# Performance work log

Measured on AMD Instinct MI355X. Metric: run time of the kernel, lower is better.

Reference implementation:

```python
import jax, jax.numpy as jnp
import numpy as np
import math
from jax import lax

# cfg['MODEL'] constants
MU = 0.1          # FISTA step size
LMBD = 0.1        # LAMBDA[0], sparsity weight
N_DICT = 1        # EXPANSION_FACTOR
N_STEPS = 6       # NUM_LAYERS (FISTA iterations)
K = 3             # kernel_size
PAD = 1           # padding
STRIDE = 1        # stride (POOLING=False, stride passed to conv)
DN = ('NCHW', 'OIHW', 'NCHW')


def _conv(x, w):
    # F.conv2d(x, w, stride=1, padding=PAD)
    return lax.conv_general_dilated(x, w, (STRIDE, STRIDE), [(PAD, PAD), (PAD, PAD)], dimension_numbers=DN)


def _conv_t(y, w):
    # F.conv_transpose2d(y, w, stride=1, padding=PAD) == conv2d with flipped, in/out-swapped kernel, pad K-1-PAD
    wt = jnp.transpose(jnp.flip(w, (-1, -2)), (1, 0, 2, 3))  # [Cin, Cout, K, K]
    p = K - 1 - PAD
    return lax.conv_general_dilated(y, wt, (1, 1), [(p, p), (p, p)], dimension_numbers=DN)


def _shrink(z, thr):
    # non_negative=True soft-threshold: relu(z - thr)
    return jax.nn.relu(z - thr)


def setup_inputs() -> dict:
    key = jax.random.key(0)
    k1, k2 = jax.random.split(key)
    x = jax.random.normal(k1, (16, 64, 56, 56), dtype=jnp.float32)
    # dictionary weight [out_channels, in_channels*n_dict, K, K], kaiming-ish scale
    W = jax.random.normal(k2, (128, 64 * N_DICT, K, K), dtype=jnp.float32) * 0.05
    return {"x": x, "W": W}


def reference(x, W):
    # w_norm: each output filter normalized to unit Frobenius norm
    Wn = W / jnp.sqrt(jnp.sum(W * W, axis=(1, 2, 3), keepdims=True) + 1e-12)
    thr = MU * LMBD
    xr = jnp.tile(x, (1, N_DICT, 1, 1)) if N_DICT > 1 else x

    # FISTA iteration 0: c = shrink(mu * D^T x)
    c = _shrink(MU * _conv(xr, Wn), thr)
    y = c
    c_prev = c
    t = 1.0
    for _ in range(N_STEPS - 1):
        r = xr - _conv_t(y, Wn)                       # residual x - D c
        c_new = _shrink(y + MU * _conv(r, Wn), thr)   # gradient step + shrink
        t_next = (1.0 + math.sqrt(1.0 + 4.0 * t * t)) / 2.0
        y = c_new + ((t - 1.0) / t_next) * (c_new - c_prev)  # momentum
        c_prev = c_new
        t = t_next
    # POOLING=False -> DictConv2d returns the sparse code directly
    return c_prev
```

## Files before the change

### kernel.cpp

```cpp
#include <hip/hip_runtime.h>
#include <hip/hip_bf16.h>
#include <math.h>

typedef __attribute__((ext_vector_type(8))) short short8;
typedef __attribute__((ext_vector_type(4))) float f32x4;

#define MU_  0.1f
#define THR_ 0.01f

static __device__ inline short f2bf(float f) {
    __hip_bfloat16 h = __float2bfloat16(f);
    return *reinterpret_cast<short*>(&h);
}
static __device__ inline float bf2f(unsigned short u) {
    unsigned int x = ((unsigned int)u) << 16;
    return __builtin_bit_cast(float, x);
}

#define ZB_ 5916

__global__ __launch_bounds__(256) void prep_kernel(
    const float* __restrict__ x, const float* __restrict__ W,
    float4* __restrict__ zbase, int n4,
    short* __restrict__ Xp, short* __restrict__ Wf2, short* __restrict__ Wt2) {
    __shared__ float lx[64 * 57];
    const int bid = blockIdx.x, tid = threadIdx.x;
    if (bid < ZB_) {
        int i = bid * 256 + tid;
        if (i < n4) zbase[i] = make_float4(0.f, 0.f, 0.f, 0.f);
    } else if (bid < ZB_ + 32) {
        int co = (bid - ZB_) * 4 + (tid >> 6);
        int ci = tid & 63;
        const float* wp = W + (co * 64 + ci) * 9;
        float v[9]; float s = 0.f;
#pragma unroll
        for (int t = 0; t < 9; ++t) { v[t] = wp[t]; s += v[t] * v[t]; }
#pragma unroll
        for (int off = 32; off; off >>= 1) s += __shfl_xor(s, off, 64);
        float inv = 1.0f / sqrtf(s + 1e-12f);
#pragma unroll
        for (int t = 0; t < 9; ++t) {
            Wf2[((t * 8 + (ci >> 3)) * 128 + co) * 8 + (ci & 7)] = f2bf(v[t] * inv);
            Wt2[((t * 16 + (co >> 3)) * 64 + ci) * 8 + (co & 7)] = f2bf(v[8 - t] * inv);
        }
    } else {
        int pb = bid - ZB_ - 32;
        int row = pb % 58, n = pb / 58;
        short* dst = Xp + ((size_t)(n * 58 + row) * 68) * 64;
        if (row >= 1 && row <= 56) {
            int h = row - 1;
            for (int j = tid; j < 64 * 56; j += 256) {
                int ci = j / 56, w = j - ci * 56;
                lx[ci * 57 + w] = x[((size_t)(n * 64 + ci)) * 3136 + h * 56 + w];
            }
            __syncthreads();
            for (int j = tid; j < 68 * 64; j += 256) {
                int s = j >> 6, ci = j & 63;
                float val = (s >= 2 && s < 58) ? lx[ci * 57 + (s - 2)] : 0.f;
                dst[(s << 6) + (ci ^ ((s & 7) << 3))] = f2bf(val);
            }
        } else {
            for (int j = tid; j < 68 * 64; j += 256) dst[j] = 0;
        }
    }
}

__global__ __launch_bounds__(256, 4) void conv_fwd(
    const short* __restrict__ inp,
    const short* __restrict__ Wf2,
    short* __restrict__ Yp,
    short* __restrict__ Cp,
    float* __restrict__ outp, int mode, float beta) {
    __shared__ __align__(16) short smem[14688];
    const int bid = blockIdx.x, tid = threadIdx.x;
    const int sid = (bid & 7) * 112 + (bid >> 3);
    const int n = sid / 56, r = sid - n * 56 + 1;
    {
        const short8* src = (const short8*)(inp + ((size_t)(n * 58 + (r - 1)) * 68) * 64);
        for (int j = tid; j < 1632; j += 256) {
            int srow = j >> 3, w = j & 7;
            *(short8*)(smem + srow * 72 + w * 8) = src[j];
        }
    }
    const int lane = tid & 63, ct = tid >> 6, quad = lane >> 4, l15 = lane & 15;
    const int cog = ct & 1, pxg = ct >> 1;
    const size_t prow = ((size_t)(n * 58 + r) * 68) * 128;

    short8 yold8[2], cold8[2];
    int pvv[2], pg[2]; bool pok[2];
#pragma unroll
    for (int k = 0; k < 2; ++k) {
        int item = tid + k * 256;
        pok[k] = item < 448;
        pvv[k] = item >> 3; pg[k] = item & 7;
        if (mode != 0 && pok[k]) {
            int s = pvv[k] + 2;
            size_t off = prow + (size_t)s * 128 + 8 * (pg[k] ^ (s & 7));
            yold8[k] = *(const short8*)(Yp + off);
            if (mode == 1) cold8[k] = *(const short8*)(Cp + off);
        }
    }
    __syncthreads();

    f32x4 acc[2][4];
#pragma unroll
    for (int pt = 0; pt < 2; ++pt)
#pragma unroll
        for (int cot = 0; cot < 4; ++cot) acc[pt][cot] = (f32x4){0.f, 0.f, 0.f, 0.f};

#pragma unroll
    for (int f = 0; f < 18; ++f) {
        const int t = f >> 1, half = f & 1;
        const int dh = t / 3, dw = t % 3;
        const int u = l15 + dw + 1;
        const int phys = (half * 4 + quad) ^ (u & 7);
        short8 areg[4];
#pragma unroll
        for (int cot = 0; cot < 4; ++cot) {
            const int co = cog * 64 + cot * 16 + l15;
            areg[cot] = *(const short8*)(Wf2 +
                ((size_t)((t * 8 + half * 4 + quad) * 128 + co)) * 8);
        }
#pragma unroll
        for (int pt = 0; pt < 2; ++pt) {
            const int pti = pxg * 2 + pt;
            const short8 bv = *(const short8*)(smem +
                (dh * 68 + pti * 16 + u) * 72 + phys * 8);
#pragma unroll
            for (int cot = 0; cot < 4; ++cot)
                acc[pt][cot] = __builtin_amdgcn_mfma_f32_16x16x32_bf16(areg[cot], bv, acc[pt][cot], 0, 0, 0);
        }
    }

    __syncthreads();
    short* tb_y = smem;
    short* tb_c = smem + 4608;
    const int h = r - 1;
#pragma unroll
    for (int hh = 0; hh < 2; ++hh) {
        if (mode != 0) {
#pragma unroll
            for (int k = 0; k < 2; ++k) if (pok[k]) {
                int o = pvv[k] * 72 + 8 * (pg[k] ^ (pvv[k] & 3));
                *(short8*)(tb_y + o) = yold8[k];
                if (mode == 1) *(short8*)(tb_c + o) = cold8[k];
            }
        }
        __syncthreads();
        if (hh == 0 && mode != 0) {
#pragma unroll
            for (int k = 0; k < 2; ++k) if (pok[k]) {
                int s = pvv[k] + 2;
                size_t off = prow + (size_t)s * 128 + 8 * ((pg[k] + 8) ^ (s & 7));
                yold8[k] = *(const short8*)(Yp + off);
                if (mode == 1) cold8[k] = *(const short8*)(Cp + off);
            }
        }
        if (cog == hh) {
#pragma unroll
            for (int pt = 0; pt < 2; ++pt) {
                const int px = pxg * 32 + pt * 16 + l15;
#pragma unroll
                for (int cot = 0; cot < 4; ++cot) {
#pragma unroll
                    for (int reg = 0; reg < 4; ++reg) {
                        const int lch = cot * 16 + quad * 4 + reg;
                        const int slot = px * 72 + (lch ^ ((px & 3) << 3));
                        const float a = acc[pt][cot][reg];
                        if (mode == 0) {
                            float c = fmaxf(MU_ * a - THR_, 0.f);
                            short cb16 = f2bf(c);
                            tb_y[slot] = cb16;
                            tb_c[slot] = cb16;
                        } else if (mode == 1) {
                            float yold = bf2f((unsigned short)tb_y[slot]);
                            float cold = bf2f((unsigned short)tb_c[slot]);
                            float c = fmaxf(yold + MU_ * a - THR_, 0.f);
                            tb_y[slot] = f2bf(c + beta * (c - cold));
                            tb_c[slot] = f2bf(c);
                        } else {
                            if (px < 56) {
                                float yold = bf2f((unsigned short)tb_y[slot]);
                                float c = fmaxf(yold + MU_ * a - THR_, 0.f);
                                outp[((size_t)(n * 128 + hh * 64 + lch)) * 3136 + h * 56 + px] = c;
                            }
                        }
                    }
                }
            }
        }
        if (mode != 2) {
            __syncthreads();
            for (int item = tid; item < 448; item += 256) {
                int vv = item >> 3, g = item & 7;
                int so = vv * 72 + 8 * (g ^ (vv & 3));
                short8 yv = *(const short8*)(tb_y + so);
                short8 cv = *(const short8*)(tb_c + so);
                int s = vv + 2;
                size_t off = prow + (size_t)s * 128 + 8 * ((g + 8 * hh) ^ (s & 7));
                *(short8*)(Yp + off) = yv;
                *(short8*)(Cp + off) = cv;
            }
        }
        if (hh == 0) __syncthreads();
    }
}

__global__ __launch_bounds__(256, 4) void conv_t(
    const short* __restrict__ Ypb,
    const short* __restrict__ Wt2,
    const short* __restrict__ Xp,
    short* __restrict__ Rp) {
    __shared__ __align__(16) short smem[14688];
    const int bid = blockIdx.x, tid = threadIdx.x;
    const int sid = (bid & 7) * 112 + (bid >> 3);
    const int n = sid / 56, r = sid - n * 56 + 1;
    const int lane = tid & 63, ct = tid >> 6, quad = lane >> 4, l15 = lane & 15;
    const short8* src = (const short8*)(Ypb + ((size_t)(n * 58 + (r - 1)) * 68) * 128);
    const size_t prow = ((size_t)(n * 58 + r) * 68) * 64;

    short8 xold8[2];
    int pvv[2], pg[2]; bool pok[2];
#pragma unroll
    for (int k = 0; k < 2; ++k) {
        int item = tid + k * 256;
        pok[k] = item < 448;
        pvv[k] = item >> 3; pg[k] = item & 7;
        if (pok[k]) {
            int s = pvv[k] + 2;
            xold8[k] = *(const short8*)(Xp + prow + (size_t)s * 64 + 8 * (pg[k] ^ (s & 7)));
        }
    }

    f32x4 acc[4];
#pragma unroll
    for (int cit = 0; cit < 4; ++cit) acc[cit] = (f32x4){0.f, 0.f, 0.f, 0.f};

#pragma unroll
    for (int p = 0; p < 2; ++p) {
        if (p) __syncthreads();
        for (int j = tid; j < 1632; j += 256) {
            int srow = j >> 3, w = j & 7;
            *(short8*)(smem + srow * 72 + w * 8) = src[srow * 16 + p * 8 + w];
        }
        __syncthreads();
#pragma unroll
        for (int f = 0; f < 18; ++f) {
            const int t = f >> 1, sh = f & 1;
            const int dh = t / 3, dw = t % 3;
            const int u = l15 + dw + 1;
            const int phys = (sh * 4 + quad) ^ (u & 7);
            short8 areg[4];
#pragma unroll
            for (int cit = 0; cit < 4; ++cit) {
                const int ci = cit * 16 + l15;
                areg[cit] = *(const short8*)(Wt2 +
                    ((size_t)((t * 16 + (p * 2 + sh) * 4 + quad) * 64 + ci)) * 8);
            }
            const short8 bv = *(const short8*)(smem +
                (dh * 68 + ct * 16 + u) * 72 + phys * 8);
#pragma unroll
            for (int cit = 0; cit < 4; ++cit)
                acc[cit] = __builtin_amdgcn_mfma_f32_16x16x32_bf16(areg[cit], bv, acc[cit], 0, 0, 0);
        }
    }

    __syncthreads();
    short* tb = smem;
#pragma unroll
    for (int k = 0; k < 2; ++k) if (pok[k]) {
        *(short8*)(tb + pvv[k] * 72 + 8 * (pg[k] ^ (pvv[k] & 3))) = xold8[k];
    }
    __syncthreads();
    {
        const int px = ct * 16 + l15;
#pragma unroll
        for (int cit = 0; cit < 4; ++cit) {
#pragma unroll
            for (int reg = 0; reg < 4; ++reg) {
                const int cir = cit * 16 + quad * 4 + reg;
                const int slot = px * 72 + (cir ^ ((px & 3) << 3));
                float xo = bf2f((unsigned short)tb[slot]);
                tb[slot] = f2bf(xo - acc[cit][reg]);
            }
        }
    }
    __syncthreads();
    for (int item = tid; item < 448; item += 256) {
        int vv = item >> 3, g = item & 7;
        short8 val = *(const short8*)(tb + vv * 72 + 8 * (g ^ (vv & 3)));
        int s = vv + 2;
        *(short8*)(Rp + prow + (size_t)s * 64 + 8 * (g ^ (s & 7))) = val;
    }
}

extern "C" void kernel_launch(void* const* d_in, const int* in_sizes, int n_in,
                              void* d_out, int out_size, void* d_ws, size_t ws_size,
                              hipStream_t stream) {
    const float* x = (const float*)d_in[0];
    const float* W = (const float*)d_in[1];
    float* out = (float*)d_out;

    const size_t XPN = (size_t)16 * 58 * 68 * 64;
    const size_t YPN = 2 * XPN;
    short* Xp = (short*)d_ws;
    short* Rp = Xp + XPN;
    short* Yp = Rp + XPN;
    short* Cp = Yp + YPN;
    short* Wf2 = Cp + YPN;
    short* Wt2 = Wf2 + 73728;

    const int n4 = (int)((XPN + YPN) * 2 / 16);
    const int prep_blocks = ZB_ + 32 + 58 * 16;
    hipLaunchKernelGGL(prep_kernel, dim3(prep_blocks), dim3(256), 0, stream,
                       x, W, (float4*)Rp, n4, Xp, Wf2, Wt2);

    dim3 b(256, 1, 1);
    hipLaunchKernelGGL(conv_fwd, dim3(896), b, 0, stream, Xp, Wf2, Yp, Cp,
                       (float*)nullptr, 0, 0.f);
    double t = 1.0;
    for (int it = 1; it <= 5; ++it) {
        hipLaunchKernelGGL(conv_t, dim3(896), b, 0, stream, Yp, Wt2, Xp, Rp);
        double tn = (1.0 + sqrt(1.0 + 4.0 * t * t)) / 2.0;
        float beta = (float)((t - 1.0) / tn);
        hipLaunchKernelGGL(conv_fwd, dim3(896), b, 0, stream, Rp, Wf2, Yp, Cp,
                           (it == 5) ? out : (float*)nullptr, (it == 5) ? 2 : 1,
                           beta);
        t = tn;
    }
}
```

Measured before the change: 358.4 us.

## Fuse transposed conv and forward conv with halo recompute and ping-pong Y buffers

Replaces the separate conv_t and conv_fwd launches per FISTA step with one kernel. Each block recomputes the residual for its three needed rows into shared memory, then runs the forward conv and shrink/momentum update. Y is ping-ponged between two buffers to avoid read/write hazards. This removes the residual's global round trip and a launch per iteration. In exchange it triples the transposed-conv work, halves occupancy, and doubles shared memory use.

Result: slower. 1.259 ms (+251.4%).

```diff
diff --git a/kernel.cpp b/kernel.cpp
--- a/kernel.cpp
+++ b/kernel.cpp
@@ -7,6 +7,7 @@
 
 #define MU_  0.1f
 #define THR_ 0.01f
+#define ZB_  7888
 
 static __device__ inline short f2bf(float f) {
     __hip_bfloat16 h = __float2bfloat16(f);
@@ -16,8 +17,6 @@
     unsigned int x = ((unsigned int)u) << 16;
     return __builtin_bit_cast(float, x);
 }
-
-#define ZB_ 5916
 
 __global__ __launch_bounds__(256) void prep_kernel(
     const float* __restrict__ x, const float* __restrict__ W,
@@ -69,8 +68,7 @@
     const short* __restrict__ inp,
     const short* __restrict__ Wf2,
     short* __restrict__ Yp,
-    short* __restrict__ Cp,
-    float* __restrict__ outp, int mode, float beta) {
+    short* __restrict__ Cp) {
     __shared__ __align__(16) short smem[14688];
     const int bid = blockIdx.x, tid = threadIdx.x;
     const int sid = (bid & 7) * 112 + (bid >> 3);
@@ -85,21 +83,6 @@
     const int lane = tid & 63, ct = tid >> 6, quad = lane >> 4, l15 = lane & 15;
     const int cog = ct & 1, pxg = ct >> 1;
     const size_t prow = ((size_t)(n * 58 + r) * 68) * 128;
-
-    short8 yold8[2], cold8[2];
-    int pvv[2], pg[2]; bool pok[2];
-#pragma unroll
-    for (int k = 0; k < 2; ++k) {
-        int item = tid + k * 256;
-        pok[k] = item < 448;
-        pvv[k] = item >> 3; pg[k] = item & 7;
-        if (mode != 0 && pok[k]) {
-            int s = pvv[k] + 2;
-            size_t off = prow + (size_t)s * 128 + 8 * (pg[k] ^ (s & 7));
-            yold8[k] = *(const short8*)(Yp + off);
-            if (mode == 1) cold8[k] = *(const short8*)(Cp + off);
-        }
-    }
     __syncthreads();
 
     f32x4 acc[2][4];
@@ -135,27 +118,8 @@
     __syncthreads();
     short* tb_y = smem;
     short* tb_c = smem + 4608;
-    const int h = r - 1;
 #pragma unroll
     for (int hh = 0; hh < 2; ++hh) {
-        if (mode != 0) {
-#pragma unroll
-            for (int k = 0; k < 2; ++k) if (pok[k]) {
-                int o = pvv[k] * 72 + 8 * (pg[k] ^ (pvv[k] & 3));
-                *(short8*)(tb_y + o) = yold8[k];
-                if (mode == 1) *(short8*)(tb_c + o) = cold8[k];
-            }
-        }
-        __syncthreads();
-        if (hh == 0 && mode != 0) {
-#pragma unroll
-            for (int k = 0; k < 2; ++k) if (pok[k]) {
-                int s = pvv[k] + 2;
-                size_t off = prow + (size_t)s * 128 + 8 * ((pg[k] + 8) ^ (s & 7));
-                yold8[k] = *(const short8*)(Yp + off);
-                if (mode == 1) cold8[k] = *(const short8*)(Cp + off);
-            }
-        }
         if (cog == hh) {
 #pragma unroll
             for (int pt = 0; pt < 2; ++pt) {
@@ -166,13 +130,212 @@
                     for (int reg = 0; reg < 4; ++reg) {
                         const int lch = cot * 16 + quad * 4 + reg;
                         const int slot = px * 72 + (lch ^ ((px & 3) << 3));
-                        const float a = acc[pt][cot][reg];
-                        if (mode == 0) {
-                            float c = fmaxf(MU_ * a - THR_, 0.f);
-                            short cb16 = f2bf(c);
-                            tb_y[slot] = cb16;
-                            tb_c[slot] = cb16;
-                        } else if (mode == 1) {
+                        float c = fmaxf(MU_ * acc[pt][cot][reg] - THR_, 0.f);
+                        short cb16 = f2bf(c);
+                        tb_y[slot] = cb16;
+                        tb_c[slot] = cb16;
+                    }
+                }
+            }
+        }
+        __syncthreads();
+        for (int item = tid; item < 448; item += 256) {
+            int vv = item >> 3, g = item & 7;
+            int so = vv * 72 + 8 * (g ^ (vv & 3));
+            short8 yv = *(const short8*)(tb_y + so);
+            short8 cv = *(const short8*)(tb_c + so);
+            int s = vv + 2;
+            size_t off = prow + (size_t)s * 128 + 8 * ((g + 8 * hh) ^ (s & 7));
+            *(short8*)(Yp + off) = yv;
+            *(short8*)(Cp + off) = cv;
+        }
+        if (hh == 0) __syncthreads();
+    }
+}
+
+__global__ __launch_bounds__(256, 2) void conv_fused(
+    const short* __restrict__ Ycur,
+    const short* __restrict__ Wt2,
+    const short* __restrict__ Wf2,
+    const short* __restrict__ Xp,
+    short* __restrict__ Ynext,
+    short* __restrict__ Cp,
+    float* __restrict__ outp, int mode, float beta) {
+    __shared__ __align__(16) short smem[29376];
+    short* Ybuf  = smem;
+    short* Rtile = smem + 14688;
+    const int bid = blockIdx.x, tid = threadIdx.x;
+    const int sid = (bid & 7) * 112 + (bid >> 3);
+    const int n = sid / 56, r = sid - n * 56 + 1;
+    const int lane = tid & 63, ct = tid >> 6, quad = lane >> 4, l15 = lane & 15;
+
+    for (int j = tid; j < 1836; j += 256)
+        ((short8*)Rtile)[j] = (short8){0, 0, 0, 0, 0, 0, 0, 0};
+
+    for (int rr_i = 0; rr_i < 3; ++rr_i) {
+        const int rr = r - 1 + rr_i;
+        if (rr < 1 || rr > 56) continue;
+        const short8* src = (const short8*)(Ycur + ((size_t)(n * 58 + (rr - 1)) * 68) * 128);
+        const size_t xrow = ((size_t)(n * 58 + rr) * 68) * 64;
+
+        short8 xold8[2];
+        int pvv[2], pg[2]; bool pok[2];
+#pragma unroll
+        for (int k = 0; k < 2; ++k) {
+            int item = tid + k * 256;
+            pok[k] = item < 448;
+            pvv[k] = item >> 3; pg[k] = item & 7;
+            if (pok[k]) {
+                int s = pvv[k] + 2;
+                xold8[k] = *(const short8*)(Xp + xrow + (size_t)s * 64 + 8 * (pg[k] ^ (s & 7)));
+            }
+        }
+
+        f32x4 acc[4];
+#pragma unroll
+        for (int cit = 0; cit < 4; ++cit) acc[cit] = (f32x4){0.f, 0.f, 0.f, 0.f};
+
+#pragma unroll
+        for (int p = 0; p < 2; ++p) {
+            __syncthreads();
+            for (int j = tid; j < 1632; j += 256) {
+                int srow = j >> 3, w = j & 7;
+                *(short8*)(Ybuf + srow * 72 + w * 8) = src[srow * 16 + p * 8 + w];
+            }
+            __syncthreads();
+#pragma unroll
+            for (int f = 0; f < 18; ++f) {
+                const int t = f >> 1, sh = f & 1;
+                const int dh = t / 3, dw = t % 3;
+                const int u = l15 + dw + 1;
+                const int phys = (sh * 4 + quad) ^ (u & 7);
+                short8 areg[4];
+#pragma unroll
+                for (int cit = 0; cit < 4; ++cit) {
+                    const int ci = cit * 16 + l15;
+                    areg[cit] = *(const short8*)(Wt2 +
+                        ((size_t)((t * 16 + (p * 2 + sh) * 4 + quad) * 64 + ci)) * 8);
+                }
+                const short8 bv = *(const short8*)(Ybuf +
+                    (dh * 68 + ct * 16 + u) * 72 + phys * 8);
+#pragma unroll
+                for (int cit = 0; cit < 4; ++cit)
+                    acc[cit] = __builtin_amdgcn_mfma_f32_16x16x32_bf16(areg[cit], bv, acc[cit], 0, 0, 0);
+            }
+        }
+
+        __syncthreads();
+        short* tb = Ybuf;
+#pragma unroll
+        for (int k = 0; k < 2; ++k) if (pok[k]) {
+            *(short8*)(tb + pvv[k] * 72 + 8 * (pg[k] ^ (pvv[k] & 3))) = xold8[k];
+        }
+        __syncthreads();
+        {
+            const int px = ct * 16 + l15;
+#pragma unroll
+            for (int cit = 0; cit < 4; ++cit) {
+#pragma unroll
+                for (int reg = 0; reg < 4; ++reg) {
+                    const int cir = cit * 16 + quad * 4 + reg;
+                    const int slot = px * 72 + (cir ^ ((px & 3) << 3));
+                    float xo = bf2f((unsigned short)tb[slot]);
+                    tb[slot] = f2bf(xo - acc[cit][reg]);
+                }
+            }
+        }
+        __syncthreads();
+        for (int item = tid; item < 448; item += 256) {
+            int vv = item >> 3, g = item & 7;
+            short8 val = *(const short8*)(tb + vv * 72 + 8 * (g ^ (vv & 3)));
+            int s = vv + 2;
+            *(short8*)(Rtile + (size_t)(rr_i * 68 + s) * 72 + 8 * (g ^ (s & 7))) = val;
+        }
+    }
+
+    const int cog = ct & 1, pxg = ct >> 1;
+    const size_t prow = ((size_t)(n * 58 + r) * 68) * 128;
+
+    short8 yold8[2], cold8[2];
+    int qvv[2], qg[2]; bool qok[2];
+#pragma unroll
+    for (int k = 0; k < 2; ++k) {
+        int item = tid + k * 256;
+        qok[k] = item < 448;
+        qvv[k] = item >> 3; qg[k] = item & 7;
+        if (qok[k]) {
+            int s = qvv[k] + 2;
+            size_t off = prow + (size_t)s * 128 + 8 * (qg[k] ^ (s & 7));
+            yold8[k] = *(const short8*)(Ycur + off);
+            if (mode == 1) cold8[k] = *(const short8*)(Cp + off);
+        }
+    }
+    __syncthreads();
+
+    f32x4 facc[2][4];
+#pragma unroll
+    for (int pt = 0; pt < 2; ++pt)
+#pragma unroll
+        for (int cot = 0; cot < 4; ++cot) facc[pt][cot] = (f32x4){0.f, 0.f, 0.f, 0.f};
+
+#pragma unroll
+    for (int f = 0; f < 18; ++f) {
+        const int t = f >> 1, half = f & 1;
+        const int dh = t / 3, dw = t % 3;
+        const int u = l15 + dw + 1;
+        const int phys = (half * 4 + quad) ^ (u & 7);
+        short8 areg[4];
+#pragma unroll
+        for (int cot = 0; cot < 4; ++cot) {
+            const int co = cog * 64 + cot * 16 + l15;
+            areg[cot] = *(const short8*)(Wf2 +
+                ((size_t)((t * 8 + half * 4 + quad) * 128 + co)) * 8);
+        }
+#pragma unroll
+        for (int pt = 0; pt < 2; ++pt) {
+            const int pti = pxg * 2 + pt;
+            const short8 bv = *(const short8*)(Rtile +
+                (dh * 68 + pti * 16 + u) * 72 + phys * 8);
+#pragma unroll
+            for (int cot = 0; cot < 4; ++cot)
+                facc[pt][cot] = __builtin_amdgcn_mfma_f32_16x16x32_bf16(areg[cot], bv, facc[pt][cot], 0, 0, 0);
+        }
+    }
+
+    __syncthreads();
+    short* tb_y = Ybuf;
+    short* tb_c = Ybuf + 4608;
+    const int h = r - 1;
+#pragma unroll
+    for (int hh = 0; hh < 2; ++hh) {
+#pragma unroll
+        for (int k = 0; k < 2; ++k) if (qok[k]) {
+            int o = qvv[k] * 72 + 8 * (qg[k] ^ (qvv[k] & 3));
+            *(short8*)(tb_y + o) = yold8[k];
+            if (mode == 1) *(short8*)(tb_c + o) = cold8[k];
+        }
+        __syncthreads();
+        if (hh == 0) {
+#pragma unroll
+            for (int k = 0; k < 2; ++k) if (qok[k]) {
+                int s = qvv[k] + 2;
+                size_t off = prow + (size_t)s * 128 + 8 * ((qg[k] + 8) ^ (s & 7));
+                yold8[k] = *(const short8*)(Ycur + off);
+                if (mode == 1) cold8[k] = *(const short8*)(Cp + off);
+            }
+        }
+        if (cog == hh) {
+#pragma unroll
+            for (int pt = 0; pt < 2; ++pt) {
+                const int px = pxg * 32 + pt * 16 + l15;
+#pragma unroll
+                for (int cot = 0; cot < 4; ++cot) {
+#pragma unroll
+                    for (int reg = 0; reg < 4; ++reg) {
+                        const int lch = cot * 16 + quad * 4 + reg;
+                        const int slot = px * 72 + (lch ^ ((px & 3) << 3));
+                        const float a = facc[pt][cot][reg];
+                        if (mode == 1) {
                             float yold = bf2f((unsigned short)tb_y[slot]);
                             float cold = bf2f((unsigned short)tb_c[slot]);
                             float c = fmaxf(yold + MU_ * a - THR_, 0.f);
@@ -189,7 +352,7 @@
                 }
             }
         }
-        if (mode != 2) {
+        if (mode == 1) {
             __syncthreads();
             for (int item = tid; item < 448; item += 256) {
                 int vv = item >> 3, g = item & 7;
@@ -198,99 +361,11 @@
                 short8 cv = *(const short8*)(tb_c + so);
                 int s = vv + 2;
                 size_t off = prow + (size_t)s * 128 + 8 * ((g + 8 * hh) ^ (s & 7));
-                *(short8*)(Yp + off) = yv;
+                *(short8*)(Ynext + off) = yv;
                 *(short8*)(Cp + off) = cv;
             }
         }
         if (hh == 0) __syncthreads();
-    }
-}
-
-__global__ __launch_bounds__(256, 4) void conv_t(
-    const short* __restrict__ Ypb,
-    const short* __restrict__ Wt2,
-    const short* __restrict__ Xp,
-    short* __restrict__ Rp) {
-    __shared__ __align__(16) short smem[14688];
-    const int bid = blockIdx.x, tid = threadIdx.x;
-    const int sid = (bid & 7) * 112 + (bid >> 3);
-    const int n = sid / 56, r = sid - n * 56 + 1;
-    const int lane = tid & 63, ct = tid >> 6, quad = lane >> 4, l15 = lane & 15;
-    const short8* src = (const short8*)(Ypb + ((size_t)(n * 58 + (r - 1)) * 68) * 128);
-    const size_t prow = ((size_t)(n * 58 + r) * 68) * 64;
-
-    short8 xold8[2];
-    int pvv[2], pg[2]; bool pok[2];
-#pragma unroll
-    for (int k = 0; k < 2; ++k) {
-        int item = tid + k * 256;
-        pok[k] = item < 448;
-        pvv[k] = item >> 3; pg[k] = item & 7;
-        if (pok[k]) {
-            int s = pvv[k] + 2;
-            xold8[k] = *(const short8*)(Xp + prow + (size_t)s * 64 + 8 * (pg[k] ^ (s & 7)));
-        }
-    }
-
-    f32x4 acc[4];
-#pragma unroll
-    for (int cit = 0; cit < 4; ++cit) acc[cit] = (f32x4){0.f, 0.f, 0.f, 0.f};
-
-#pragma unroll
-    for (int p = 0; p < 2; ++p) {
-        if (p) __syncthreads();
-        for (int j = tid; j < 1632; j += 256) {
-            int srow = j >> 3, w = j & 7;
-            *(short8*)(smem + srow * 72 + w * 8) = src[srow * 16 + p * 8 + w];
-        }
-        __syncthreads();
-#pragma unroll
-        for (int f = 0; f < 18; ++f) {
-            const int t = f >> 1, sh = f & 1;
-            const int dh = t / 3, dw = t % 3;
-            const int u = l15 + dw + 1;
-            const int phys = (sh * 4 + quad) ^ (u & 7);
-            short8 areg[4];
-#pragma unroll
-            for (int cit = 0; cit < 4; ++cit) {
-                const int ci = cit * 16 + l15;
-                areg[cit] = *(const short8*)(Wt2 +
-                    ((size_t)((t * 16 + (p * 2 + sh) * 4 + quad) * 64 + ci)) * 8);
-            }
-            const short8 bv = *(const short8*)(smem +
-                (dh * 68 + ct * 16 + u) * 72 + phys * 8);
-#pragma unroll
-            for (int cit = 0; cit < 4; ++cit)
-                acc[cit] = __builtin_amdgcn_mfma_f32_16x16x32_bf16(areg[cit], bv, acc[cit], 0, 0, 0);
-        }
-    }
-
-    __syncthreads();
-    short* tb = smem;
-#pragma unroll
-    for (int k = 0; k < 2; ++k) if (pok[k]) {
-        *(short8*)(tb + pvv[k] * 72 + 8 * (pg[k] ^ (pvv[k] & 3))) = xold8[k];
-    }
-    __syncthreads();
-    {
-        const int px = ct * 16 + l15;
-#pragma unroll
-        for (int cit = 0; cit < 4; ++cit) {
-#pragma unroll
-            for (int reg = 0; reg < 4; ++reg) {
-                const int cir = cit * 16 + quad * 4 + reg;
-                const int slot = px * 72 + (cir ^ ((px & 3) << 3));
-                float xo = bf2f((unsigned short)tb[slot]);
-                tb[slot] = f2bf(xo - acc[cit][reg]);
-            }
-        }
-    }
-    __syncthreads();
-    for (int item = tid; item < 448; item += 256) {
-        int vv = item >> 3, g = item & 7;
-        short8 val = *(const short8*)(tb + vv * 72 + 8 * (g ^ (vv & 3)));
-        int s = vv + 2;
-        *(short8*)(Rp + prow + (size_t)s * 64 + 8 * (g ^ (s & 7))) = val;
     }
 }
 
@@ -304,28 +379,29 @@
     const size_t XPN = (size_t)16 * 58 * 68 * 64;
     const size_t YPN = 2 * XPN;
     short* Xp = (short*)d_ws;
-    short* Rp = Xp + XPN;
-    short* Yp = Rp + XPN;
-    short* Cp = Yp + YPN;
+    short* YA = Xp + XPN;
+    short* YB = YA + YPN;
+    short* Cp = YB + YPN;
     short* Wf2 = Cp + YPN;
     short* Wt2 = Wf2 + 73728;
 
-    const int n4 = (int)((XPN + YPN) * 2 / 16);
+    const int n4 = (int)(2 * YPN * 2 / 16);
     const int prep_blocks = ZB_ + 32 + 58 * 16;
     hipLaunchKernelGGL(prep_kernel, dim3(prep_blocks), dim3(256), 0, stream,
-                       x, W, (float4*)Rp, n4, Xp, Wf2, Wt2);
+                       x, W, (float4*)YA, n4, Xp, Wf2, Wt2);
 
     dim3 b(256, 1, 1);
-    hipLaunchKernelGGL(conv_fwd, dim3(896), b, 0, stream, Xp, Wf2, Yp, Cp,
-                       (float*)nullptr, 0, 0.f);
+    hipLaunchKernelGGL(conv_fwd, dim3(896), b, 0, stream, Xp, Wf2, YA, Cp);
     double t = 1.0;
     for (int it = 1; it <= 5; ++it) {
-        hipLaunchKernelGGL(conv_t, dim3(896), b, 0, stream, Yp, Wt2, Xp, Rp);
         double tn = (1.0 + sqrt(1.0 + 4.0 * t * t)) / 2.0;
         float beta = (float)((t - 1.0) / tn);
-        hipLaunchKernelGGL(conv_fwd, dim3(896), b, 0, stream, Rp, Wf2, Yp, Cp,
-                           (it == 5) ? out : (float*)nullptr, (it == 5) ? 2 : 1,
-                           beta);
+        short* Ycur  = (it & 1) ? YA : YB;
+        short* Ynext = (it & 1) ? YB : YA;
+        hipLaunchKernelGGL(conv_fused, dim3(896), b, 0, stream,
+                           Ycur, Wt2, Wf2, Xp, Ynext, Cp,
+                           (it == 5) ? out : (float*)nullptr,
+                           (it == 5) ? 2 : 1, beta);
         t = tn;
     }
 }
```

## Zero only padding rows, skip loading pad columns, prefetch second channel half

Applied to the files above, without the earlier changes.

The prep kernel now zeroes only the top and bottom padding rows of the residual and Y buffers, not the whole workspace. The conv kernels stop loading the padding columns from global memory and instead write zeros into those LDS slots directly. conv_t also prefetches the second channel half into registers before computing the first half, so that load overlaps MFMA work. The cost is more register pressure, plus the assumption that interior pad columns are never written by other kernels.

After: 352.2 us. About the same (-1.7%).

```diff
diff --git a/kernel.cpp b/kernel.cpp
--- a/kernel.cpp
+++ b/kernel.cpp
@@ -7,6 +7,7 @@
 
 #define MU_  0.1f
 #define THR_ 0.01f
+#define ZB_  204
 
 static __device__ inline short f2bf(float f) {
     __hip_bfloat16 h = __float2bfloat16(f);
@@ -17,17 +18,25 @@
     return __builtin_bit_cast(float, x);
 }
 
-#define ZB_ 5916
-
 __global__ __launch_bounds__(256) void prep_kernel(
     const float* __restrict__ x, const float* __restrict__ W,
-    float4* __restrict__ zbase, int n4,
+    short* __restrict__ Rp, short* __restrict__ Yp,
     short* __restrict__ Xp, short* __restrict__ Wf2, short* __restrict__ Wt2) {
     __shared__ float lx[64 * 57];
     const int bid = blockIdx.x, tid = threadIdx.x;
     if (bid < ZB_) {
-        int i = bid * 256 + tid;
-        if (i < n4) zbase[i] = make_float4(0.f, 0.f, 0.f, 0.f);
+        int gid = bid * 256 + tid;
+        const short8 z = {0, 0, 0, 0, 0, 0, 0, 0};
+        if (gid < 17408) {
+            int ridx = gid / 544, off = gid - ridx * 544;
+            int n = ridx >> 1, row = (ridx & 1) * 57;
+            ((short8*)(Rp + ((size_t)(n * 58 + row) * 68) * 64))[off] = z;
+        } else {
+            int g2 = gid - 17408;
+            int ridx = g2 / 1088, off = g2 - ridx * 1088;
+            int n = ridx >> 1, row = (ridx & 1) * 57;
+            ((short8*)(Yp + ((size_t)(n * 58 + row) * 68) * 128))[off] = z;
+        }
     } else if (bid < ZB_ + 32) {
         int co = (bid - ZB_) * 4 + (tid >> 6);
         int ci = tid & 63;
@@ -62,6 +71,16 @@
         } else {
             for (int j = tid; j < 68 * 64; j += 256) dst[j] = 0;
         }
+    }
+}
+
+static __device__ __forceinline__ void zero_lds_pads(short* smem, int tid) {
+    const short8 z = {0, 0, 0, 0, 0, 0, 0, 0};
+    for (int i = tid; i < 288; i += 256) {
+        int sr = i >> 3, w = i & 7;
+        int row = sr / 12, sl = sr - row * 12;
+        int s = (sl < 2) ? sl : sl + 56;
+        *(short8*)(smem + (row * 68 + s) * 72 + w * 8) = z;
     }
 }
 
@@ -75,11 +94,13 @@
     const int bid = blockIdx.x, tid = threadIdx.x;
     const int sid = (bid & 7) * 112 + (bid >> 3);
     const int n = sid / 56, r = sid - n * 56 + 1;
+    zero_lds_pads(smem, tid);
     {
         const short8* src = (const short8*)(inp + ((size_t)(n * 58 + (r - 1)) * 68) * 64);
-        for (int j = tid; j < 1632; j += 256) {
-            int srow = j >> 3, w = j & 7;
-            *(short8*)(smem + srow * 72 + w * 8) = src[j];
+        for (int j = tid; j < 1344; j += 256) {
+            int sr = j >> 3, w = j & 7;
+            int row = sr / 56, s = sr - row * 56 + 2;
+            *(short8*)(smem + (row * 68 + s) * 72 + w * 8) = src[(row * 68 + s) * 8 + w];
         }
     }
     const int lane = tid & 63, ct = tid >> 6, quad = lane >> 4, l15 = lane & 15;
@@ -232,18 +253,45 @@
         }
     }
 
+    zero_lds_pads(smem, tid);
+    for (int j = tid; j < 1344; j += 256) {
+        int sr = j >> 3, w = j & 7;
+        int row = sr / 56, s = sr - row * 56 + 2;
+        *(short8*)(smem + (row * 68 + s) * 72 + w * 8) = src[(row * 68 + s) * 16 + w];
+    }
+
     f32x4 acc[4];
 #pragma unroll
     for (int cit = 0; cit < 4; ++cit) acc[cit] = (f32x4){0.f, 0.f, 0.f, 0.f};
 
+    __syncthreads();
+
+    short8 pf[6];
+#pragma unroll
+    for (int k = 0; k < 6; ++k) {
+        int j = tid + k * 256;
+        if (j < 1344) {
+            int sr = j >> 3, w = j & 7;
+            int row = sr / 56, s = sr - row * 56 + 2;
+            pf[k] = src[(row * 68 + s) * 16 + 8 + w];
+        }
+    }
+
 #pragma unroll
     for (int p = 0; p < 2; ++p) {
-        if (p) __syncthreads();
-        for (int j = tid; j < 1632; j += 256) {
-            int srow = j >> 3, w = j & 7;
-            *(short8*)(smem + srow * 72 + w * 8) = src[srow * 16 + p * 8 + w];
-        }
-        __syncthreads();
+        if (p) {
+            __syncthreads();
+#pragma unroll
+            for (int k = 0; k < 6; ++k) {
+                int j = tid + k * 256;
+                if (j < 1344) {
+                    int sr = j >> 3, w = j & 7;
+                    int row = sr / 56, s = sr - row * 56 + 2;
+                    *(short8*)(smem + (row * 68 + s) * 72 + w * 8) = pf[k];
+                }
+            }
+            __syncthreads();
+        }
 #pragma unroll
         for (int f = 0; f < 18; ++f) {
             const int t = f >> 1, sh = f & 1;
@@ -310,10 +358,9 @@
     short* Wf2 = Cp + YPN;
     short* Wt2 = Wf2 + 73728;
 
-    const int n4 = (int)((XPN + YPN) * 2 / 16);
     const int prep_blocks = ZB_ + 32 + 58 * 16;
     hipLaunchKernelGGL(prep_kernel, dim3(prep_blocks), dim3(256), 0, stream,
-                       x, W, (float4*)Rp, n4, Xp, Wf2, Wt2);
+                       x, W, Rp, Yp, Xp, Wf2, Wt2);
 
     dim3 b(256, 1, 1);
     hipLaunchKernelGGL(conv_fwd, dim3(896), b, 0, stream, Xp, Wf2, Yp, Cp,
```
